# Optimization experiments

Measured on AMD Instinct MI355X. Metric: run time of the kernel, lower is better.

## Reference

```python
import jax, jax.numpy as jnp
import numpy as np

NUM_HEAD = 8
ATTN_DIM = 512
WINDOW_WIDTH = 31
HALF_WIN = WINDOW_WIDTH // 2  # symmetric band half-width
NEG_INF = -1e10


def setup_inputs() -> dict:
    key = jax.random.key(0)
    k0, k1, k2 = jax.random.split(key, 3)
    n, c, w = 4, 512, 2048
    out_dim = 512
    input_ = jax.random.normal(k0, (n, c, 1, w), dtype=jnp.float32)
    mask = jnp.ones((n, w), dtype=jnp.float32)  # 1 = valid key position
    # xavier-uniform-like init for the two linears, zero bias (as in the module)
    lim_in = np.sqrt(6.0 / (c + 3 * ATTN_DIM)).astype(np.float32)
    W_in = jax.random.uniform(k1, (3 * ATTN_DIM, c), jnp.float32, -lim_in, lim_in)
    b_in = jnp.zeros((3 * ATTN_DIM,), jnp.float32)
    lim_fc = np.sqrt(6.0 / (ATTN_DIM + out_dim)).astype(np.float32)
    W_fc = jax.random.uniform(k2, (out_dim, ATTN_DIM), jnp.float32, -lim_fc, lim_fc)
    b_fc = jnp.zeros((out_dim,), jnp.float32)
    return {"input_": input_, "mask": mask, "W_in": W_in, "b_in": b_in,
            "W_fc": W_fc, "b_fc": b_fc}


def reference(input_, mask, W_in, b_in, W_fc, b_fc):
    n, c, h, w = input_.shape  # h == 1
    d = ATTN_DIM // NUM_HEAD
    x = input_.reshape(n, c, w).transpose(0, 2, 1)          # [n, w, c]
    temp = x @ W_in.T + b_in                                # [n, w, 3A]
    temp = temp.transpose(0, 2, 1)                          # [n, 3A, w]
    # channel layout after chunk(num_head) then chunk(3): [h, {q,k,v}, d]
    qkv = temp.reshape(n, NUM_HEAD, 3, d, w)
    q, k, v = qkv[:, :, 0], qkv[:, :, 1], qkv[:, :, 2]      # each [n, H, d, w]
    scale = NUM_HEAD / ATTN_DIM                              # == 1/d_head
    attn = jnp.einsum('nhdi,nhdj->nhij', q, k) * scale       # [n, H, w, w]
    # windowed band mask combined with per-key padding mask (clip_mask/mha_mask)
    idx = jnp.arange(w)
    band = jnp.abs(idx[:, None] - idx[None, :]) <= HALF_WIN  # [w, w]
    valid = band[None, None, :, :] & (mask > 0.5)[:, None, None, :]
    attn = jnp.where(valid, attn, NEG_INF)                   # pre-softmax mask
    attn = jax.nn.softmax(attn, axis=-1)
    attn = jnp.where(valid, attn, 0.0)                       # post-softmax mask
    # dropout in eval mode (identity) for a deterministic reference
    out = jnp.einsum('nhdj,nhij->nhdi', v, attn)             # [n, H, d, w]
    out = out.reshape(n, ATTN_DIM, w).transpose(0, 2, 1)     # [n, w, A]
    out = out @ W_fc.T + b_fc                                # [n, w, out_dim]
    od = out.shape[-1]
    return out.transpose(0, 2, 1).reshape(n, od, 1, w)
```

## Files before the change

kernel.cpp:

```cpp
#include <hip/hip_runtime.h>
#include <hip/hip_bf16.h>
#include <math.h>

#define W_SEQ   2048
#define C_IN    512
#define N_BATCH 4
#define NHEAD   8
#define QKV_CH  1536
#define OUT_CH  512
#define ATTND   512
#define N1_4    (QKV_CH * C_IN / 4)
#define N2_4    (OUT_CH * ATTND / 4)

typedef __attribute__((ext_vector_type(8))) short bf16x8;
typedef __attribute__((ext_vector_type(8))) unsigned short u16x8;
typedef __attribute__((ext_vector_type(4))) float f32x4;

__device__ __forceinline__ void gld16(const void* g, void* l) {
    __builtin_amdgcn_global_load_lds((const __attribute__((address_space(1))) void*)g,
                                     (__attribute__((address_space(3))) void*)l, 16, 0, 0);
}
__device__ __forceinline__ unsigned short f2bf(float f) {
    unsigned u = __float_as_uint(f);
    return (unsigned short)((u + 0x7FFFu + ((u >> 16) & 1u)) >> 16);
}
__device__ __forceinline__ unsigned ld_flag(const unsigned* p) {
    return __hip_atomic_load(p, __ATOMIC_RELAXED, __HIP_MEMORY_SCOPE_AGENT);
}


__device__ __forceinline__ void prep_unit(char* sm, int b,
    const float* __restrict__ input, unsigned short* __restrict__ Xh,
    const float* __restrict__ W_in, unsigned short* __restrict__ Winh,
    const float* __restrict__ W_fc, unsigned short* __restrict__ Wfch)
{
    const int t = threadIdx.x;
    float (*ts)[65] = (float(*)[65])sm;
    const int n  = b >> 8, rm = b & 255;
    const int i0 = (rm & 31) * 64, c0 = (rm >> 5) * 64;
    const int tx = t & 63, ty = t >> 6;
    #pragma unroll
    for (int s = 0; s < 16; ++s) {
        const int c = s * 4 + ty;
        ts[c][tx] = input[((size_t)(n * C_IN + c0 + c)) * W_SEQ + i0 + tx];
    }
    __syncthreads();
    const int c8 = t & 7, il = t >> 3;
    #pragma unroll
    for (int s = 0; s < 2; ++s) {
        const int i = il + 32 * s;
        u16x8 hv;
        #pragma unroll
        for (int e = 0; e < 8; ++e) hv[e] = f2bf(ts[c8 * 8 + e][i]);
        *(u16x8*)(&Xh[((size_t)(n * W_SEQ + i0 + i)) * C_IN + c0 + c8 * 8]) = hv;
    }
    const int idx = b * 256 + t;
    if (idx < N1_4) {
        const float4 v = ((const float4*)W_in)[idx];
        ushort4 hh; hh.x = f2bf(v.x); hh.y = f2bf(v.y); hh.z = f2bf(v.z); hh.w = f2bf(v.w);
        ((ushort4*)Winh)[idx] = hh;
    } else {
        const int j = idx - N1_4;
        const float4 v = ((const float4*)W_fc)[j];
        ushort4 hh; hh.x = f2bf(v.x); hh.y = f2bf(v.y); hh.z = f2bf(v.z); hh.w = f2bf(v.w);
        ((ushort4*)Wfch)[j] = hh;
    }
}

template<int EPI>
__device__ __forceinline__ void gemm_body(char* sm, int bx, int by,
    const unsigned short* __restrict__ A, const unsigned short* __restrict__ B,
    const float* __restrict__ bias, void* __restrict__ Cv, const int ldc)
{
    const int t = threadIdx.x;
    const int l = t & 63, w = t >> 6;
    const int m0 = by * 128, n0 = bx * 128;
    const int wm = w >> 1, wn = w & 1;

    const int subrow = l >> 3;
    const int swz    = ((l & 7) ^ subrow) << 4;
    const char* pA = (const char*)A + (size_t)m0 * 1024 + swz;
    const char* pB = (const char*)B + (size_t)n0 * 1024 + swz;

    const int frow = l & 15;
    f32x4 acc[4][4] = {};

    for (int k0 = 0; k0 < 512; k0 += 64) {
        const int kb = k0 * 2;
        #pragma unroll
        for (int c = 0; c < 4; ++c) {
            const int q = 4 * w + c;
            const size_t roff = (size_t)(q * 8 + subrow) * 1024 + kb;
            gld16(pA + roff, sm +         q * 1024);
            gld16(pB + roff, sm + 16384 + q * 1024);
        }
        __syncthreads();
        #pragma unroll
        for (int kk = 0; kk < 2; ++kk) {
            const int cswz = (kk * 64 + ((l >> 4) << 4)) ^ ((l & 7) << 4);
            bf16x8 a[4], b[4];
            #pragma unroll
            for (int mi = 0; mi < 4; ++mi)
                a[mi] = *(const bf16x8*)(sm + (wm * 64 + mi * 16 + frow) * 128 + cswz);
            #pragma unroll
            for (int ni = 0; ni < 4; ++ni)
                b[ni] = *(const bf16x8*)(sm + 16384 + (wn * 64 + ni * 16 + frow) * 128 + cswz);
            #pragma unroll
            for (int mi = 0; mi < 4; ++mi)
                #pragma unroll
                for (int ni = 0; ni < 4; ++ni)
                    acc[mi][ni] = __builtin_amdgcn_mfma_f32_16x16x32_bf16(a[mi], b[ni], acc[mi][ni], 0, 0, 0);
        }
        __syncthreads();
    }

    const int g = l >> 4;
    int cols[4]; float bcol[4];
    #pragma unroll
    for (int ni = 0; ni < 4; ++ni) {
        cols[ni] = n0 + wn * 64 + ni * 16 + frow;
        bcol[ni] = (EPI == 0) ? bias[cols[ni]] : 0.f;
    }
    #pragma unroll
    for (int mi = 0; mi < 4; ++mi) {
        #pragma unroll
        for (int r = 0; r < 4; ++r) {
            const int rowg = m0 + wm * 64 + mi * 16 + g * 4 + r;
            float brow = 0.f;
            if (EPI == 1) brow = bias[rowg];
            #pragma unroll
            for (int ni = 0; ni < 4; ++ni) {
                const float v = acc[mi][ni][r];
                if (EPI == 0) {
                    ((unsigned short*)Cv)[(size_t)rowg * ldc + cols[ni]] = f2bf(v + bcol[ni]);
                } else {
                    const int nb = cols[ni] >> 11, ii = cols[ni] & (W_SEQ - 1);
                    ((float*)Cv)[((size_t)(nb * OUT_CH + rowg)) * W_SEQ + ii] = v + brow;
                }
            }
        }
    }
}

#define VT_OFF  13824
#define MSK_OFF 30208

__device__ __forceinline__ void attn_body(char* sm, int blk,
    const unsigned short* __restrict__ qkv, const float* __restrict__ mask,
    unsigned short* __restrict__ aoh)
{
    const int t = threadIdx.x, l = t & 63, w = t >> 6;
    const int i0 = (blk & 31) * 64, h = (blk >> 5) & 7, n = blk >> 8;
    const int lr = l & 15, lg = l >> 4;

    const char* tb = (const char*)qkv + ((size_t)n * W_SEQ * QKV_CH + h * 192) * 2;

    const int r8 = l >> 3, c8 = l & 7;
    #pragma unroll
    for (int it = 0; it < 3; ++it) {
        const int jl = w * 24 + it * 8 + r8;
        const int jg = i0 - 16 + jl;
        bf16x8 vv = {};
        if (jg >= 0 && jg < W_SEQ)
            vv = *(const bf16x8*)(tb + (size_t)jg * 3072 + 256 + c8 * 16);
        const int J0 = jl >> 3;
        #pragma unroll
        for (int e = 0; e < 8; ++e) {
            const int d = c8 * 8 + e;
            const int fold = ((d >> 3) ^ d) & 7;
            *(unsigned short*)(sm + VT_OFF + d * 256 + (((J0 ^ fold) << 4) | ((jl & 7) * 2)))
                = (unsigned short)vv[e];
        }
    }
    bf16x8 qh[2];
    {
        const char* qrow = tb + (size_t)(i0 + w * 16 + lr) * 3072 + lg * 16;
        qh[0] = *(const bf16x8*)(qrow);
        qh[1] = *(const bf16x8*)(qrow + 64);
    }
    if (t < 96) {
        const int jg = i0 - 16 + t;
        *(float*)(sm + MSK_OFF + t * 4) = (jg >= 0 && jg < W_SEQ) ? mask[n * W_SEQ + jg] : 0.f;
    }

    f32x4 sacc[6] = {};
    __builtin_amdgcn_s_setprio(1);
    #pragma unroll
    for (int nf = 0; nf < 6; ++nf) {
        const int jl = nf * 16 + lr;
        const int jg = i0 - 16 + jl;
        const bool inr = (jg >= 0) && (jg < W_SEQ);
        const char* kp = tb + (size_t)jg * 3072 + 128;
        #pragma unroll
        for (int kk = 0; kk < 2; ++kk) {
            bf16x8 kh = {};
            if (inr) kh = *(const bf16x8*)(kp + kk * 64 + lg * 16);
            sacc[nf] = __builtin_amdgcn_mfma_f32_16x16x32_bf16(qh[kk], kh, sacc[nf], 0, 0, 0);
        }
    }
    __builtin_amdgcn_s_setprio(0);
    __syncthreads();

    float mv[6];
    #pragma unroll
    for (int nf = 0; nf < 6; ++nf)
        mv[nf] = *(const float*)(sm + MSK_OFF + (nf * 16 + lr) * 4);

    #pragma unroll
    for (int r = 0; r < 4; ++r) {
        const int ri = w * 16 + lg * 4 + r;
        float sv[6], ls = 0.f;
        #pragma unroll
        for (int nf = 0; nf < 6; ++nf) {
            const int jcol = nf * 16 + lr;
            const bool valid = (jcol > ri) && (jcol <= ri + 31) && (mv[nf] > 0.5f);
            const float p = valid ? __expf(sacc[nf][r] * 0.015625f) : 0.f;
            sv[nf] = p;
            ls += p;
        }
        #pragma unroll
        for (int off = 1; off <= 8; off <<= 1) ls += __shfl_xor(ls, off);
        const float rinv = (ls > 0.f) ? 1.f / ls : 0.f;
        #pragma unroll
        for (int nf = 0; nf < 6; ++nf)
            *(unsigned short*)(sm + ri * 208 + (nf * 16 + lr) * 2) = f2bf(sv[nf] * rinv);
    }

    f32x4 oacc[4] = {};
    __builtin_amdgcn_s_setprio(1);
    #pragma unroll
    for (int ks = 0; ks < 3; ++ks) {
        const bf16x8 pah = *(const bf16x8*)(sm + (w * 16 + lr) * 208 + ks * 64 + lg * 16);
        #pragma unroll
        for (int nf2 = 0; nf2 < 4; ++nf2) {
            const int dd = nf2 * 16 + lr;
            const int fold = ((dd >> 3) ^ dd) & 7;
            const bf16x8 vb = *(const bf16x8*)(sm + VT_OFF + dd * 256 + (((4 * ks + lg) ^ fold) << 4));
            oacc[nf2] = __builtin_amdgcn_mfma_f32_16x16x32_bf16(pah, vb, oacc[nf2], 0, 0, 0);
        }
    }
    __builtin_amdgcn_s_setprio(0);

    #pragma unroll
    for (int nf2 = 0; nf2 < 4; ++nf2) {
        #pragma unroll
        for (int r = 0; r < 4; ++r) {
            const int ri = w * 16 + lg * 4 + r;
            aoh[((size_t)(n * W_SEQ + i0 + ri)) * ATTND + h * 64 + nf2 * 16 + lr] = f2bf(oacc[nf2][r]);
        }
    }
}

__global__ __launch_bounds__(256, 4) void fused_all_k(
    const float* __restrict__ input, const float* __restrict__ mask,
    const float* __restrict__ W_in,  const float* __restrict__ b_in,
    const float* __restrict__ W_fc,  const float* __restrict__ b_fc,
    float* __restrict__ out,
    unsigned short* __restrict__ QKVh, unsigned short* __restrict__ AOh,
    unsigned short* __restrict__ Winh, unsigned short* __restrict__ Wfch,
    unsigned short* __restrict__ Xh, unsigned* __restrict__ flg)
{
    __shared__ __align__(16) char sm[32768];
    const int b = blockIdx.x;
    unsigned* xdone  = flg;
    unsigned* wpanel = flg + 1024;
    unsigned* wfc    = flg + 1280;
    unsigned* qdone  = flg + 2048;
    unsigned* adone  = flg + 3072;

    prep_unit(sm, b, input, Xh, W_in, Winh, W_fc, Wfch);
    __syncthreads();
    if (threadIdx.x == 0) {
        __threadfence();
        atomicAdd(xdone + ((b >> 8) * 16 + ((b & 31) >> 1)) * 16, 1u);
        if (b < 768) atomicAdd(wpanel + (b >> 6) * 16, 1u);
        else         atomicAdd(wfc, 1u);
    }

    if (b < 768) {
        const int y8 = b & 7, r = b >> 3;
        const int bx = r % 12;
        const int by = (((r / 12) + 6) & 7) * 8 + y8;
        if (threadIdx.x == 0) {
            while (ld_flag(wpanel + bx * 16) < 64u) __builtin_amdgcn_s_sleep(2);
            while (ld_flag(xdone  + by * 16) < 16u) __builtin_amdgcn_s_sleep(2);
            __threadfence();
        }
        __syncthreads();
        gemm_body<0>(sm, bx, by, Xh, Winh, b_in, QKVh, QKV_CH);
        __syncthreads();
        if (threadIdx.x == 0) {
            __threadfence();
            atomicAdd(qdone + by * 16, 1u);
        }
    }

    {
        const int n = b >> 8, i0 = (b & 31) * 64;
        const int row1 = n * W_SEQ + ((i0 >= 16) ? i0 - 16 : 0);
        const int row2 = n * W_SEQ + ((i0 + 79 <= W_SEQ - 1) ? i0 + 79 : W_SEQ - 1);
        const int t1 = row1 >> 7, t2 = row2 >> 7;
        if (threadIdx.x == 0) {
            while (ld_flag(qdone + t1 * 16) < 12u) __builtin_amdgcn_s_sleep(2);
            while (ld_flag(qdone + t2 * 16) < 12u) __builtin_amdgcn_s_sleep(2);
            __threadfence();
        }
        __syncthreads();
        attn_body(sm, b, QKVh, mask, AOh);
        __syncthreads();
        if (threadIdx.x == 0) {
            __threadfence();
            const int panel = n * 16 + (i0 >> 7);
            atomicAdd(adone + panel * 16, 1u);
        }
    }

    if (b < 256) {
        const int bx = b >> 2, by = b & 3;
        if (threadIdx.x == 0) {
            while (ld_flag(wfc) < 256u) __builtin_amdgcn_s_sleep(2);
            while (ld_flag(adone + bx * 16) < 16u) __builtin_amdgcn_s_sleep(2);
            __threadfence();
        }
        __syncthreads();
        gemm_body<1>(sm, bx, by, Wfch, AOh, b_fc, out, 0);
    }
}

__global__ __launch_bounds__(256, 4) void prep_sep_k(
    const float* __restrict__ input, unsigned short* __restrict__ Xh,
    const float* __restrict__ W_in, unsigned short* __restrict__ Winh,
    const float* __restrict__ W_fc, unsigned short* __restrict__ Wfch)
{
    __shared__ __align__(16) char sm[32768];
    prep_unit(sm, blockIdx.x, input, Xh, W_in, Winh, W_fc, Wfch);
}
__global__ __launch_bounds__(256, 4) void gemm1_sep_k(
    const unsigned short* __restrict__ A, const unsigned short* __restrict__ B,
    const float* __restrict__ bias, unsigned short* __restrict__ C)
{
    __shared__ __align__(16) char sm[32768];
    const int d = blockIdx.x, y8 = d & 7, r = d >> 3;
    gemm_body<0>(sm, r % 12, (((r / 12) + 6) & 7) * 8 + y8, A, B, bias, C, QKV_CH);
}
__global__ __launch_bounds__(256, 4) void attn_sep_k(
    const unsigned short* __restrict__ qkv, const float* __restrict__ mask,
    unsigned short* __restrict__ aoh)
{
    __shared__ __align__(16) char sm[32768];
    attn_body(sm, blockIdx.x, qkv, mask, aoh);
}
__global__ __launch_bounds__(256, 4) void gemm2_sep_k(
    const unsigned short* __restrict__ A, const unsigned short* __restrict__ B,
    const float* __restrict__ bias, float* __restrict__ out)
{
    __shared__ __align__(16) char sm[32768];
    gemm_body<1>(sm, blockIdx.x >> 2, blockIdx.x & 3, A, B, bias, out, 0);
}

extern "C" void kernel_launch(void* const* d_in, const int* in_sizes, int n_in,
                              void* d_out, int out_size, void* d_ws, size_t ws_size,
                              hipStream_t stream)
{
    const float* input = (const float*)d_in[0];
    const float* mask  = (const float*)d_in[1];
    const float* W_in  = (const float*)d_in[2];
    const float* b_in  = (const float*)d_in[3];
    const float* W_fc  = (const float*)d_in[4];
    const float* b_fc  = (const float*)d_in[5];
    float* out = (float*)d_out;
    char* ws = (char*)d_ws;

    unsigned short* QKVh = (unsigned short*)ws;
    unsigned short* AOh  = (unsigned short*)(ws + 25165824);
    unsigned short* Winh = (unsigned short*)(ws + 33554432);
    unsigned short* Wfch = (unsigned short*)(ws + 35127296);
    unsigned short* Xh   = (unsigned short*)(ws + 35651584);
    unsigned*       flg  = (unsigned*)(ws + 46137344);

    int occ = 0;
    hipOccupancyMaxActiveBlocksPerMultiprocessor(&occ, fused_all_k, 256, 0);

    if (occ >= 4) {
        hipMemsetAsync(flg, 0, 16384, stream);
        fused_all_k<<<dim3(1024), 256, 0, stream>>>(
            input, mask, W_in, b_in, W_fc, b_fc, out,
            QKVh, AOh, Winh, Wfch, Xh, flg);
    } else {
        prep_sep_k <<<dim3(1024), 256, 0, stream>>>(input, Xh, W_in, Winh, W_fc, Wfch);
        gemm1_sep_k<<<dim3(768),  256, 0, stream>>>(Xh, Winh, b_in, QKVh);
        attn_sep_k <<<dim3(1024), 256, 0, stream>>>(QKVh, mask, AOh);
        gemm2_sep_k<<<dim3(256),  256, 0, stream>>>(Wfch, AOh, b_fc, out);
    }
}
```

Measured before the change: 53.01 us.

## Load GEMM A fragments directly to registers and stage attention K tile in LDS

In the GEMM body, the A operand fragments now come straight from global memory into registers, and only B is staged through LDS. This halves LDS traffic and shared-memory footprint per k-step. In the attention body, K rows for the window are loaded cooperatively into a padded LDS tile together with V, replacing per-wave redundant global loads of K. The cost is an extra barrier and possibly uncoalesced, latency-exposed global loads for A.

```diff
diff --git a/kernel.cpp b/kernel.cpp
--- a/kernel.cpp
+++ b/kernel.cpp
@@ -14,6 +14,7 @@
 
 typedef __attribute__((ext_vector_type(8))) short bf16x8;
 typedef __attribute__((ext_vector_type(8))) unsigned short u16x8;
+typedef __attribute__((ext_vector_type(4))) short s16x4;
 typedef __attribute__((ext_vector_type(4))) float f32x4;
 
 __device__ __forceinline__ void gld16(const void* g, void* l) {
@@ -79,10 +80,14 @@
 
     const int subrow = l >> 3;
     const int swz    = ((l & 7) ^ subrow) << 4;
-    const char* pA = (const char*)A + (size_t)m0 * 1024 + swz;
     const char* pB = (const char*)B + (size_t)n0 * 1024 + swz;
 
-    const int frow = l & 15;
+    const int frow = l & 15, lg = l >> 4;
+    const char* pAr[4];
+    #pragma unroll
+    for (int mi = 0; mi < 4; ++mi)
+        pAr[mi] = (const char*)A + (size_t)(m0 + wm * 64 + mi * 16 + frow) * 1024 + lg * 16;
+
     f32x4 acc[4][4] = {};
 
     for (int k0 = 0; k0 < 512; k0 += 64) {
@@ -90,31 +95,32 @@
         #pragma unroll
         for (int c = 0; c < 4; ++c) {
             const int q = 4 * w + c;
-            const size_t roff = (size_t)(q * 8 + subrow) * 1024 + kb;
-            gld16(pA + roff, sm +         q * 1024);
-            gld16(pB + roff, sm + 16384 + q * 1024);
-        }
-        __syncthreads();
-        #pragma unroll
-        for (int kk = 0; kk < 2; ++kk) {
-            const int cswz = (kk * 64 + ((l >> 4) << 4)) ^ ((l & 7) << 4);
-            bf16x8 a[4], b[4];
+            gld16(pB + (size_t)(q * 8 + subrow) * 1024 + kb, sm + q * 1024);
+        }
+        bf16x8 a[2][4];
+        #pragma unroll
+        for (int kk = 0; kk < 2; ++kk)
             #pragma unroll
             for (int mi = 0; mi < 4; ++mi)
-                a[mi] = *(const bf16x8*)(sm + (wm * 64 + mi * 16 + frow) * 128 + cswz);
+                a[kk][mi] = *(const bf16x8*)(pAr[mi] + kb + kk * 64);
+        __syncthreads();
+        #pragma unroll
+        for (int kk = 0; kk < 2; ++kk) {
+            const int cswz = (kk * 64 + (lg << 4)) ^ ((l & 7) << 4);
+            bf16x8 b[4];
             #pragma unroll
             for (int ni = 0; ni < 4; ++ni)
-                b[ni] = *(const bf16x8*)(sm + 16384 + (wn * 64 + ni * 16 + frow) * 128 + cswz);
+                b[ni] = *(const bf16x8*)(sm + (wn * 64 + ni * 16 + frow) * 128 + cswz);
             #pragma unroll
             for (int mi = 0; mi < 4; ++mi)
                 #pragma unroll
                 for (int ni = 0; ni < 4; ++ni)
-                    acc[mi][ni] = __builtin_amdgcn_mfma_f32_16x16x32_bf16(a[mi], b[ni], acc[mi][ni], 0, 0, 0);
-        }
-        __syncthreads();
-    }
-
-    const int g = l >> 4;
+                    acc[mi][ni] = __builtin_amdgcn_mfma_f32_16x16x32_bf16(a[kk][mi], b[ni], acc[mi][ni], 0, 0, 0);
+        }
+        __syncthreads();
+    }
+
+    const int g = lg;
     int cols[4]; float bcol[4];
     #pragma unroll
     for (int ni = 0; ni < 4; ++ni) {
@@ -160,9 +166,13 @@
     for (int it = 0; it < 3; ++it) {
         const int jl = w * 24 + it * 8 + r8;
         const int jg = i0 - 16 + jl;
-        bf16x8 vv = {};
-        if (jg >= 0 && jg < W_SEQ)
-            vv = *(const bf16x8*)(tb + (size_t)jg * 3072 + 256 + c8 * 16);
+        bf16x8 kv = {}, vv = {};
+        if (jg >= 0 && jg < W_SEQ) {
+            const char* rp = tb + (size_t)jg * 3072;
+            kv = *(const bf16x8*)(rp + 128 + c8 * 16);
+            vv = *(const bf16x8*)(rp + 256 + c8 * 16);
+        }
+        *(bf16x8*)(sm + jl * 144 + c8 * 16) = kv;
         const int J0 = jl >> 3;
         #pragma unroll
         for (int e = 0; e < 8; ++e) {
@@ -182,19 +192,15 @@
         const int jg = i0 - 16 + t;
         *(float*)(sm + MSK_OFF + t * 4) = (jg >= 0 && jg < W_SEQ) ? mask[n * W_SEQ + jg] : 0.f;
     }
+    __syncthreads();
 
     f32x4 sacc[6] = {};
     __builtin_amdgcn_s_setprio(1);
     #pragma unroll
     for (int nf = 0; nf < 6; ++nf) {
-        const int jl = nf * 16 + lr;
-        const int jg = i0 - 16 + jl;
-        const bool inr = (jg >= 0) && (jg < W_SEQ);
-        const char* kp = tb + (size_t)jg * 3072 + 128;
         #pragma unroll
         for (int kk = 0; kk < 2; ++kk) {
-            bf16x8 kh = {};
-            if (inr) kh = *(const bf16x8*)(kp + kk * 64 + lg * 16);
+            const bf16x8 kh = *(const bf16x8*)(sm + (nf * 16 + lr) * 144 + kk * 64 + lg * 16);
             sacc[nf] = __builtin_amdgcn_mfma_f32_16x16x32_bf16(qh[kk], kh, sacc[nf], 0, 0, 0);
         }
     }
```

After: 83.60 us. 1.58x slower.
